# Kernel optimization log

Measured on AMD Instinct MI355X. Metric: run time of the kernel, lower is better.

The kernel has to match this reference:

```python
import jax, jax.numpy as jnp
import numpy as np

N_NODES = 100000
N_EDGES = 1600000
NUM_FEATURES = 512
HIDDEN = 128
NUM_CLASSES = 40


def setup_inputs() -> dict:
    key = jax.random.key(0)
    ks = jax.random.split(key, 6)
    x = jax.random.normal(ks[0], (N_NODES, NUM_FEATURES), dtype=jnp.float32)
    edge_index = jax.random.randint(ks[1], (2, N_EDGES), 0, N_NODES, dtype=jnp.int32)
    W1 = jax.random.normal(ks[2], (NUM_FEATURES, HIDDEN), dtype=jnp.float32) * 0.05
    b1 = jnp.zeros((HIDDEN,), dtype=jnp.float32)
    W2 = jax.random.normal(ks[3], (HIDDEN, NUM_CLASSES), dtype=jnp.float32) * 0.05
    b2 = jnp.zeros((NUM_CLASSES,), dtype=jnp.float32)
    return {"x": x, "edge_index": edge_index, "W1": W1, "b1": b1, "W2": W2, "b2": b2}


def _gcn_conv(x, W, b, src, dst, n):
    # PyG GCNConv: h = W x; out = D^{-1/2} (A + I) D^{-1/2} h + b
    h = x @ W                                            # [N, out]
    deg = jax.ops.segment_sum(jnp.ones(src.shape[0], h.dtype), dst,
                              num_segments=n) + 1.0      # +1 for self loop
    inv_sqrt = jax.lax.rsqrt(deg)                        # [N]
    coef = inv_sqrt[src] * inv_sqrt[dst]                 # [E]
    msgs = h[src] * coef[:, None]                        # [E, out] gather
    agg = jax.ops.segment_sum(msgs, dst, num_segments=n) # scatter-add
    agg = agg + h * (inv_sqrt * inv_sqrt)[:, None]       # self-loop term
    return agg + b


def reference(x, edge_index, W1, b1, W2, b2):
    src, dst = edge_index[0], edge_index[1]
    n = x.shape[0]
    h = jax.nn.relu(_gcn_conv(x, W1, b1, src, dst, n))
    # F.dropout(training=self.training): eval mode -> identity
    out = _gcn_conv(h, W2, b2, src, dst, n)
    return jax.nn.log_softmax(out, axis=1)
```

## Files before the change

kernel.cpp:

```cpp
#include <hip/hip_runtime.h>
#include <hip/hip_bf16.h>
#include <math.h>

#define N_NODES 100000
#define N_EDGES 1600000
#define F_IN 512
#define HID 128
#define NCLS 40
#define DEG_CAP 64
#define GM 128
#define NGB 782

typedef __attribute__((ext_vector_type(8))) short short8;
typedef __attribute__((ext_vector_type(4))) float floatx4;

__device__ __forceinline__ unsigned short f2bf(float x) {
    unsigned u = __builtin_bit_cast(unsigned, x);
    unsigned r = (u + 0x7FFFu + ((u >> 16) & 1u)) >> 16;
    return (unsigned short)r;
}
__device__ __forceinline__ float bflo(unsigned u) {
    return __builtin_bit_cast(float, u << 16);
}
__device__ __forceinline__ float bfhi(unsigned u) {
    return __builtin_bit_cast(float, u & 0xFFFF0000u);
}
__device__ __forceinline__ float dinv(int dg) {
    return rsqrtf((float)dg + 1.0f);
}


__global__ __launch_bounds__(256) void k_prep(
    const float* __restrict__ W1, unsigned short* __restrict__ W1t,
    const float* __restrict__ W2, unsigned short* __restrict__ W2th,
    unsigned short* __restrict__ W2tl, int* __restrict__ cursor) {
    int b = blockIdx.x;
    if (b < 256) {
        int idx = b * 256 + threadIdx.x;
        int n = idx >> 9, k = idx & 511;
        W1t[idx] = f2bf(W1[k * HID + n]);
    } else if (b < 280) {
        int idx = (b - 256) * 256 + threadIdx.x;
        int n = idx >> 7, k = idx & 127;
        float v = (n < NCLS) ? W2[k * NCLS + n] : 0.f;
        unsigned short hi = f2bf(v);
        unsigned short lo = f2bf(v - bflo(hi));
        W2th[idx] = hi;
        W2tl[idx] = lo;
    } else {
        int i = (b - 280) * 256 + threadIdx.x;
        if (i < N_NODES) cursor[i] = 0;
    }
}


__global__ __launch_bounds__(256) void k_fused_g1f(
    const float* __restrict__ A,
    const unsigned short* __restrict__ Bt,
    unsigned short* __restrict__ C,
    int M,
    const int* __restrict__ src, const int* __restrict__ dst,
    int* __restrict__ cursor, int* __restrict__ csr)
{
    __shared__ unsigned short Asl[128 * 40];
    __shared__ unsigned short Bsl[128 * 40];

    if (blockIdx.x >= NGB) {
        int i = (blockIdx.x - NGB) * 256 + threadIdx.x;
        int d = dst[i];
        int pos = atomicAdd(&cursor[d], 1);
        if (pos < DEG_CAP) csr[((size_t)d << 6) + pos] = src[i];
        return;
    }

    const int tid  = threadIdx.x;
    const int wave = tid >> 6;
    const int lane = tid & 63;
    const int quad = lane >> 4;
    const int l15  = lane & 15;
    const int wm   = (wave >> 1) * 64;
    const int wn   = (wave & 1) * 64;
    const int block_m = blockIdx.x * GM;

    floatx4 acc[4][4];
    #pragma unroll
    for (int i = 0; i < 4; ++i)
        #pragma unroll
        for (int j = 0; j < 4; ++j) acc[i][j] = (floatx4){0.f, 0.f, 0.f, 0.f};

    for (int k0 = 0; k0 < F_IN; k0 += 32) {
        #pragma unroll
        for (int i = 0; i < 4; ++i) {
            int f  = tid + 256 * i;
            int r  = f >> 3;
            int kq = f & 7;
            int gr = block_m + r;
            gr = gr < M ? gr : M - 1;
            floatx4 v = *(const floatx4*)&A[(size_t)gr * F_IN + k0 + kq * 4];
            unsigned lo = (unsigned)f2bf(v.x) | ((unsigned)f2bf(v.y) << 16);
            unsigned hi = (unsigned)f2bf(v.z) | ((unsigned)f2bf(v.w) << 16);
            *(uint2*)&Asl[r * 40 + kq * 4] = make_uint2(lo, hi);
        }
        #pragma unroll
        for (int i = 0; i < 2; ++i) {
            int f  = tid + 256 * i;
            int r  = f >> 2;
            int kq = f & 3;
            int4 v = *(const int4*)&Bt[(size_t)r * F_IN + k0 + kq * 8];
            *(int4*)&Bsl[r * 40 + kq * 8] = v;
        }
        __syncthreads();

        short8 af[4], bfr[4];
        #pragma unroll
        for (int t = 0; t < 4; ++t)
            af[t] = *(const short8*)&Asl[(wm + t * 16 + l15) * 40 + quad * 8];
        #pragma unroll
        for (int t = 0; t < 4; ++t)
            bfr[t] = *(const short8*)&Bsl[(wn + t * 16 + l15) * 40 + quad * 8];

        #pragma unroll
        for (int tm = 0; tm < 4; ++tm)
            #pragma unroll
            for (int tn = 0; tn < 4; ++tn)
                acc[tm][tn] = __builtin_amdgcn_mfma_f32_16x16x32_bf16(
                    af[tm], bfr[tn], acc[tm][tn], 0, 0, 0);
        __syncthreads();
    }

    #pragma unroll
    for (int tm = 0; tm < 4; ++tm) {
        #pragma unroll
        for (int r = 0; r < 4; ++r) {
            int row = block_m + wm + tm * 16 + quad * 4 + r;
            if (row < M) {
                #pragma unroll
                for (int tn = 0; tn < 4; ++tn)
                    C[(size_t)row * HID + wn + tn * 16 + l15] =
                        f2bf(acc[tm][tn][r]);
            }
        }
    }
}


__global__ __launch_bounds__(256) void k_gather1(
    const unsigned* __restrict__ h1s,
    const int* __restrict__ deg,
    const int* __restrict__ csr,
    const float* __restrict__ b1, float* __restrict__ hrelu)
{
    const int wave = threadIdx.x >> 6;
    const int lane = threadIdx.x & 63;
    const int node = blockIdx.x * 4 + wave;
    const int start = node << 6;
    const int dgn = deg[node];
    const float invd = dinv(dgn);
    int cnt = dgn < DEG_CAP ? dgn : DEG_CAP;

    unsigned u = h1s[(size_t)node * 64 + lane];
    float acc0 = bflo(u) * invd, acc1 = bfhi(u) * invd;

    int t = 0;
    for (; t + 16 <= cnt; t += 16) {
        int4 ia = *(const int4*)&csr[start + t];
        int4 ib = *(const int4*)&csr[start + t + 4];
        int4 ic = *(const int4*)&csr[start + t + 8];
        int4 id = *(const int4*)&csr[start + t + 12];
        float w0 = dinv(deg[ia.x]), w1 = dinv(deg[ia.y]);
        float w2 = dinv(deg[ia.z]), w3 = dinv(deg[ia.w]);
        float w4 = dinv(deg[ib.x]), w5 = dinv(deg[ib.y]);
        float w6 = dinv(deg[ib.z]), w7 = dinv(deg[ib.w]);
        float w8 = dinv(deg[ic.x]), w9 = dinv(deg[ic.y]);
        float wa = dinv(deg[ic.z]), wb = dinv(deg[ic.w]);
        float wc = dinv(deg[id.x]), wd = dinv(deg[id.y]);
        float we = dinv(deg[id.z]), wf = dinv(deg[id.w]);
        unsigned u0 = h1s[(size_t)ia.x * 64 + lane];
        unsigned u1 = h1s[(size_t)ia.y * 64 + lane];
        unsigned u2 = h1s[(size_t)ia.z * 64 + lane];
        unsigned u3 = h1s[(size_t)ia.w * 64 + lane];
        unsigned u4 = h1s[(size_t)ib.x * 64 + lane];
        unsigned u5 = h1s[(size_t)ib.y * 64 + lane];
        unsigned u6 = h1s[(size_t)ib.z * 64 + lane];
        unsigned u7 = h1s[(size_t)ib.w * 64 + lane];
        unsigned u8 = h1s[(size_t)ic.x * 64 + lane];
        unsigned u9 = h1s[(size_t)ic.y * 64 + lane];
        unsigned ua = h1s[(size_t)ic.z * 64 + lane];
        unsigned ub = h1s[(size_t)ic.w * 64 + lane];
        unsigned uc = h1s[(size_t)id.x * 64 + lane];
        unsigned ud = h1s[(size_t)id.y * 64 + lane];
        unsigned ue = h1s[(size_t)id.z * 64 + lane];
        unsigned uf = h1s[(size_t)id.w * 64 + lane];
        acc0 += (bflo(u0) * w0 + bflo(u1) * w1) + (bflo(u2) * w2 + bflo(u3) * w3);
        acc1 += (bfhi(u0) * w0 + bfhi(u1) * w1) + (bfhi(u2) * w2 + bfhi(u3) * w3);
        acc0 += (bflo(u4) * w4 + bflo(u5) * w5) + (bflo(u6) * w6 + bflo(u7) * w7);
        acc1 += (bfhi(u4) * w4 + bfhi(u5) * w5) + (bfhi(u6) * w6 + bfhi(u7) * w7);
        acc0 += (bflo(u8) * w8 + bflo(u9) * w9) + (bflo(ua) * wa + bflo(ub) * wb);
        acc1 += (bfhi(u8) * w8 + bfhi(u9) * w9) + (bfhi(ua) * wa + bfhi(ub) * wb);
        acc0 += (bflo(uc) * wc + bflo(ud) * wd) + (bflo(ue) * we + bflo(uf) * wf);
        acc1 += (bfhi(uc) * wc + bfhi(ud) * wd) + (bfhi(ue) * we + bfhi(uf) * wf);
    }
    for (; t + 8 <= cnt; t += 8) {
        int4 ia = *(const int4*)&csr[start + t];
        int4 ib = *(const int4*)&csr[start + t + 4];
        float w0 = dinv(deg[ia.x]), w1 = dinv(deg[ia.y]);
        float w2 = dinv(deg[ia.z]), w3 = dinv(deg[ia.w]);
        float w4 = dinv(deg[ib.x]), w5 = dinv(deg[ib.y]);
        float w6 = dinv(deg[ib.z]), w7 = dinv(deg[ib.w]);
        unsigned u0 = h1s[(size_t)ia.x * 64 + lane];
        unsigned u1 = h1s[(size_t)ia.y * 64 + lane];
        unsigned u2 = h1s[(size_t)ia.z * 64 + lane];
        unsigned u3 = h1s[(size_t)ia.w * 64 + lane];
        unsigned u4 = h1s[(size_t)ib.x * 64 + lane];
        unsigned u5 = h1s[(size_t)ib.y * 64 + lane];
        unsigned u6 = h1s[(size_t)ib.z * 64 + lane];
        unsigned u7 = h1s[(size_t)ib.w * 64 + lane];
        acc0 += (bflo(u0) * w0 + bflo(u1) * w1) + (bflo(u2) * w2 + bflo(u3) * w3);
        acc1 += (bfhi(u0) * w0 + bfhi(u1) * w1) + (bfhi(u2) * w2 + bfhi(u3) * w3);
        acc0 += (bflo(u4) * w4 + bflo(u5) * w5) + (bflo(u6) * w6 + bflo(u7) * w7);
        acc1 += (bfhi(u4) * w4 + bfhi(u5) * w5) + (bfhi(u6) * w6 + bfhi(u7) * w7);
    }
    for (; t + 4 <= cnt; t += 4) {
        int4 ia = *(const int4*)&csr[start + t];
        float w0 = dinv(deg[ia.x]), w1 = dinv(deg[ia.y]);
        float w2 = dinv(deg[ia.z]), w3 = dinv(deg[ia.w]);
        unsigned u0 = h1s[(size_t)ia.x * 64 + lane];
        unsigned u1 = h1s[(size_t)ia.y * 64 + lane];
        unsigned u2 = h1s[(size_t)ia.z * 64 + lane];
        unsigned u3 = h1s[(size_t)ia.w * 64 + lane];
        acc0 += (bflo(u0) * w0 + bflo(u1) * w1) + (bflo(u2) * w2 + bflo(u3) * w3);
        acc1 += (bfhi(u0) * w0 + bfhi(u1) * w1) + (bfhi(u2) * w2 + bfhi(u3) * w3);
    }
    for (; t < cnt; ++t) {
        int s = csr[start + t];
        float w = dinv(deg[s]);
        unsigned uu = h1s[(size_t)s * 64 + lane];
        acc0 += bflo(uu) * w;
        acc1 += bfhi(uu) * w;
    }

    float2 b = *(const float2*)&b1[lane * 2];
    float v0 = fmaxf(acc0 * invd + b.x, 0.f);
    float v1 = fmaxf(acc1 * invd + b.y, 0.f);
    *(float2*)&hrelu[(size_t)node * HID + lane * 2] = make_float2(v0, v1);
}


#define G2M 128

__global__ __launch_bounds__(256) void k_gemm2_mfma(
    const float* __restrict__ H,
    const unsigned short* __restrict__ Bh,
    const unsigned short* __restrict__ Bl,
    const int* __restrict__ deg,
    unsigned short* __restrict__ C,
    int M)
{
    __shared__ unsigned short Ahs[128 * 40];
    __shared__ unsigned short Als[128 * 40];
    __shared__ unsigned short Bhs[48 * 136];
    __shared__ unsigned short Bls[48 * 136];

    const int tid  = threadIdx.x;
    const int wave = tid >> 6;
    const int lane = tid & 63;
    const int quad = lane >> 4;
    const int l15  = lane & 15;
    const int wm   = wave * 32;
    const int block_m = blockIdx.x * G2M;

    for (int i = tid; i < 768; i += 256) {
        int n = i >> 4;
        int k = (i & 15) * 8;
        *(int4*)&Bhs[n * 136 + k] = *(const int4*)&Bh[n * 128 + k];
        *(int4*)&Bls[n * 136 + k] = *(const int4*)&Bl[n * 128 + k];
    }

    const int ra = tid >> 3, kqa = tid & 7;
    size_t aoff[4];
    #pragma unroll
    for (int i = 0; i < 4; ++i) {
        int gr = block_m + ra + 32 * i;
        gr = gr < M ? gr : M - 1;
        aoff[i] = (size_t)gr * HID + kqa * 4;
    }

    floatx4 hreg[4];
    #pragma unroll
    for (int i = 0; i < 4; ++i) hreg[i] = *(const floatx4*)&H[aoff[i]];

    floatx4 acc[2][3];
    #pragma unroll
    for (int i = 0; i < 2; ++i)
        #pragma unroll
        for (int j = 0; j < 3; ++j) acc[i][j] = (floatx4){0.f, 0.f, 0.f, 0.f};

    for (int step = 0; step < 4; ++step) {
        #pragma unroll
        for (int i = 0; i < 4; ++i) {
            floatx4 v = hreg[i];
            unsigned short hx = f2bf(v.x), hy = f2bf(v.y);
            unsigned short hz = f2bf(v.z), hw = f2bf(v.w);
            unsigned short lx = f2bf(v.x - bflo(hx));
            unsigned short ly = f2bf(v.y - bflo(hy));
            unsigned short lz = f2bf(v.z - bflo(hz));
            unsigned short lw = f2bf(v.w - bflo(hw));
            *(uint2*)&Ahs[(ra + 32 * i) * 40 + kqa * 4] =
                make_uint2((unsigned)hx | ((unsigned)hy << 16),
                           (unsigned)hz | ((unsigned)hw << 16));
            *(uint2*)&Als[(ra + 32 * i) * 40 + kqa * 4] =
                make_uint2((unsigned)lx | ((unsigned)ly << 16),
                           (unsigned)lz | ((unsigned)lw << 16));
        }
        __syncthreads();

        if (step < 3) {
            const int k1 = (step + 1) * 32;
            #pragma unroll
            for (int i = 0; i < 4; ++i) hreg[i] = *(const floatx4*)&H[aoff[i] + k1];
        }

        const int k0 = step * 32;
        short8 ah[2], al[2], bh[3], bl[3];
        #pragma unroll
        for (int t = 0; t < 2; ++t) {
            ah[t] = *(const short8*)&Ahs[(wm + t * 16 + l15) * 40 + quad * 8];
            al[t] = *(const short8*)&Als[(wm + t * 16 + l15) * 40 + quad * 8];
        }
        #pragma unroll
        for (int t = 0; t < 3; ++t) {
            bh[t] = *(const short8*)&Bhs[(t * 16 + l15) * 136 + k0 + quad * 8];
            bl[t] = *(const short8*)&Bls[(t * 16 + l15) * 136 + k0 + quad * 8];
        }

        #pragma unroll
        for (int tm = 0; tm < 2; ++tm)
            #pragma unroll
            for (int tn = 0; tn < 3; ++tn) {
                acc[tm][tn] = __builtin_amdgcn_mfma_f32_16x16x32_bf16(
                    ah[tm], bh[tn], acc[tm][tn], 0, 0, 0);
                acc[tm][tn] = __builtin_amdgcn_mfma_f32_16x16x32_bf16(
                    al[tm], bh[tn], acc[tm][tn], 0, 0, 0);
                acc[tm][tn] = __builtin_amdgcn_mfma_f32_16x16x32_bf16(
                    ah[tm], bl[tn], acc[tm][tn], 0, 0, 0);
            }
        __syncthreads();
    }

    #pragma unroll
    for (int tm = 0; tm < 2; ++tm) {
        #pragma unroll
        for (int r = 0; r < 4; ++r) {
            int row = block_m + wm + tm * 16 + quad * 4 + r;
            if (row < M) {
                float iv = dinv(deg[row]);
                #pragma unroll
                for (int tn = 0; tn < 3; ++tn) {
                    int col = tn * 16 + l15;
                    if (col < NCLS)
                        C[(size_t)row * NCLS + col] = f2bf(acc[tm][tn][r] * iv);
                }
            }
        }
    }
}


__global__ __launch_bounds__(256) void k_gather2(
    const unsigned* __restrict__ h2s,
    const int* __restrict__ deg,
    const int* __restrict__ csr,
    const float* __restrict__ b2, float* __restrict__ out)
{
    const int wave = threadIdx.x >> 6;
    const int lane = threadIdx.x & 63;
    const int node = blockIdx.x * 4 + wave;
    const int g = lane / 20;
    const int j = lane - g * 20;
    const int start = node << 6;
    const int dgn = deg[node];
    int cnt = dgn < DEG_CAP ? dgn : DEG_CAP;

    float acc0 = 0.f, acc1 = 0.f;
    if (g == 0) {
        unsigned u = h2s[(size_t)node * 20 + j];
        acc0 = bflo(u);
        acc1 = bfhi(u);
    }
    if (g < 3) {
        int t = g;
        for (; t + 9 < cnt; t += 12) {
            int s0 = csr[start + t];
            int s1 = csr[start + t + 3];
            int s2 = csr[start + t + 6];
            int s3 = csr[start + t + 9];
            unsigned u0 = h2s[(size_t)s0 * 20 + j];
            unsigned u1 = h2s[(size_t)s1 * 20 + j];
            unsigned u2 = h2s[(size_t)s2 * 20 + j];
            unsigned u3 = h2s[(size_t)s3 * 20 + j];
            acc0 += bflo(u0) + bflo(u1);
            acc1 += bfhi(u0) + bfhi(u1);
            acc0 += bflo(u2) + bflo(u3);
            acc1 += bfhi(u2) + bfhi(u3);
        }
        for (; t + 3 < cnt; t += 6) {
            int s0 = csr[start + t];
            int s1 = csr[start + t + 3];
            unsigned u0 = h2s[(size_t)s0 * 20 + j];
            unsigned u1 = h2s[(size_t)s1 * 20 + j];
            acc0 += bflo(u0) + bflo(u1);
            acc1 += bfhi(u0) + bfhi(u1);
        }
        if (t < cnt) {
            int s = csr[start + t];
            unsigned u = h2s[(size_t)s * 20 + j];
            acc0 += bflo(u);
            acc1 += bfhi(u);
        }
    }
    acc0 += __shfl(acc0, j + 20) + __shfl(acc0, j + 40);
    acc1 += __shfl(acc1, j + 20) + __shfl(acc1, j + 40);

    float invd = dinv(dgn);
    float v0 = -INFINITY, v1 = -INFINITY;
    if (g == 0) {
        float2 b = *(const float2*)&b2[j * 2];
        v0 = acc0 * invd + b.x;
        v1 = acc1 * invd + b.y;
    }
    float m = fmaxf(v0, v1);
    #pragma unroll
    for (int mask = 16; mask; mask >>= 1) m = fmaxf(m, __shfl_xor(m, mask));
    float e = (g == 0) ? (__expf(v0 - m) + __expf(v1 - m)) : 0.f;
    #pragma unroll
    for (int mask = 16; mask; mask >>= 1) e += __shfl_xor(e, mask);
    if (g == 0) {
        float lg = __logf(e);
        *(float2*)&out[(size_t)node * NCLS + j * 2] =
            make_float2(v0 - m - lg, v1 - m - lg);
    }
}


extern "C" void kernel_launch(void* const* d_in, const int* in_sizes, int n_in,
                              void* d_out, int out_size, void* d_ws, size_t ws_size,
                              hipStream_t stream) {
    const float* x   = (const float*)d_in[0];
    const int*   ei  = (const int*)d_in[1];
    const float* W1  = (const float*)d_in[2];
    const float* b1  = (const float*)d_in[3];
    const float* W2  = (const float*)d_in[4];
    const float* b2  = (const float*)d_in[5];
    float* out = (float*)d_out;

    const int* src = ei;
    const int* dst = ei + N_EDGES;

    char* wsb = (char*)d_ws;
    float* slot1    = (float*)wsb;
    float* hrelu    = slot1 + (size_t)N_NODES * HID;
    int*   cursor   = (int*)(hrelu + (size_t)N_NODES * HID);
    int*   csr_pad  = cursor + 131072;
    unsigned short* W1t  = (unsigned short*)(csr_pad + (size_t)N_NODES * DEG_CAP);
    unsigned short* W2th = W1t + (size_t)F_IN * HID;
    unsigned short* W2tl = W2th + 48 * 128;
    unsigned short* h1s_st = (unsigned short*)slot1;
    unsigned short* h2s_st = (unsigned short*)slot1;
    unsigned* h1s_ld = (unsigned*)slot1;
    unsigned* h2s_ld = (unsigned*)slot1;

    const int T = 256;
    const int NB = (N_NODES + 255) / 256;

    k_prep<<<280 + NB, T, 0, stream>>>(W1, W1t, W2, W2th, W2tl, cursor);

    k_fused_g1f<<<NGB + N_EDGES / T, T, 0, stream>>>(
        x, W1t, h1s_st, N_NODES, src, dst, cursor, csr_pad);

    k_gather1<<<N_NODES / 4, T, 0, stream>>>(h1s_ld, cursor, csr_pad, b1, hrelu);

    k_gemm2_mfma<<<(N_NODES + G2M - 1) / G2M, T, 0, stream>>>(hrelu, W2th, W2tl, cursor, h2s_st, N_NODES);
    k_gather2<<<N_NODES / 4, T, 0, stream>>>(h2s_ld, cursor, csr_pad, b2, out);
}
```

Measured before the change: 508.5 us.

## Split CSR build into 8 cursor slices and compact per node afterwards

Edge scatter now uses eight separate per-node cursor arrays chosen by block index, each with a 16-slot sub-bucket, so concurrent atomics on the same destination spread over different addresses. A new compaction kernel uses wave ballots to pack the valid entries of each node's 128-slot row and sums the slice counts into a degree array. This is meant to cut atomic contention in the CSR build, at the cost of an extra kernel launch, twice the CSR footprint and an 8x larger cursor initialisation. The per-slice cap of 16 could drop edges on skewed degree distributions.

```diff
diff --git a/kernel.cpp b/kernel.cpp
--- a/kernel.cpp
+++ b/kernel.cpp
@@ -7,9 +7,11 @@
 #define F_IN 512
 #define HID 128
 #define NCLS 40
-#define DEG_CAP 64
 #define GM 128
 #define NGB 782
+#define NFB 6250
+#define SCAP 16
+#define CUR_N 131072
 
 typedef __attribute__((ext_vector_type(8))) short short8;
 typedef __attribute__((ext_vector_type(4))) float floatx4;
@@ -33,7 +35,7 @@
 __global__ __launch_bounds__(256) void k_prep(
     const float* __restrict__ W1, unsigned short* __restrict__ W1t,
     const float* __restrict__ W2, unsigned short* __restrict__ W2th,
-    unsigned short* __restrict__ W2tl, int* __restrict__ cursor) {
+    unsigned short* __restrict__ W2tl, int* __restrict__ cur8) {
     int b = blockIdx.x;
     if (b < 256) {
         int idx = b * 256 + threadIdx.x;
@@ -49,7 +51,7 @@
         W2tl[idx] = lo;
     } else {
         int i = (b - 280) * 256 + threadIdx.x;
-        if (i < N_NODES) cursor[i] = 0;
+        cur8[i] = 0;
     }
 }
 
@@ -60,16 +62,18 @@
     unsigned short* __restrict__ C,
     int M,
     const int* __restrict__ src, const int* __restrict__ dst,
-    int* __restrict__ cursor, int* __restrict__ csr)
+    int* __restrict__ cur8, int* __restrict__ csr)
 {
     __shared__ unsigned short Asl[128 * 40];
     __shared__ unsigned short Bsl[128 * 40];
 
     if (blockIdx.x >= NGB) {
-        int i = (blockIdx.x - NGB) * 256 + threadIdx.x;
+        int fb = blockIdx.x - NGB;
+        int i = fb * 256 + threadIdx.x;
         int d = dst[i];
-        int pos = atomicAdd(&cursor[d], 1);
-        if (pos < DEG_CAP) csr[((size_t)d << 6) + pos] = src[i];
+        int s = fb & 7;
+        int pos = atomicAdd(&cur8[s * CUR_N + d], 1);
+        if (pos < SCAP) csr[((size_t)d << 7) + s * SCAP + pos] = src[i];
         return;
     }
 
@@ -144,6 +148,42 @@
 }
 
 
+__global__ __launch_bounds__(256) void k_compact(
+    const int* __restrict__ cur8, int* __restrict__ csr, int* __restrict__ deg)
+{
+    const int wave = threadIdx.x >> 6;
+    const int lane = threadIdx.x & 63;
+    const int node = blockIdx.x * 4 + wave;
+    const size_t base = (size_t)node << 7;
+
+    int k0 = lane, k1 = lane + 64;
+    int c0 = cur8[(k0 >> 4) * CUR_N + node];
+    int c1 = cur8[(k1 >> 4) * CUR_N + node];
+    c0 = c0 < SCAP ? c0 : SCAP;
+    c1 = c1 < SCAP ? c1 : SCAP;
+    bool ok0 = (k0 & 15) < c0;
+    bool ok1 = (k1 & 15) < c1;
+
+    int v0 = csr[base + k0];
+    unsigned long long m0 = __ballot(ok0);
+    int nA = __popcll(m0);
+    int p0 = __popcll(m0 & ((1ull << lane) - 1ull));
+    if (ok0) csr[base + p0] = v0;
+
+    int v1 = csr[base + k1];
+    unsigned long long m1 = __ballot(ok1);
+    int p1 = __popcll(m1 & ((1ull << lane) - 1ull));
+    if (ok1) csr[base + nA + p1] = v1;
+
+    if (lane == 0) {
+        int dsum = 0;
+        #pragma unroll
+        for (int s = 0; s < 8; ++s) dsum += cur8[s * CUR_N + node];
+        deg[node] = dsum;
+    }
+}
+
+
 __global__ __launch_bounds__(256) void k_gather1(
     const unsigned* __restrict__ h1s,
     const int* __restrict__ deg,
@@ -153,10 +193,10 @@
     const int wave = threadIdx.x >> 6;
     const int lane = threadIdx.x & 63;
     const int node = blockIdx.x * 4 + wave;
-    const int start = node << 6;
+    const int start = node << 7;
     const int dgn = deg[node];
     const float invd = dinv(dgn);
-    int cnt = dgn < DEG_CAP ? dgn : DEG_CAP;
+    int cnt = dgn < 128 ? dgn : 128;
 
     unsigned u = h1s[(size_t)node * 64 + lane];
     float acc0 = bflo(u) * invd, acc1 = bfhi(u) * invd;
@@ -377,9 +417,9 @@
     const int node = blockIdx.x * 4 + wave;
     const int g = lane / 20;
     const int j = lane - g * 20;
-    const int start = node << 6;
+    const int start = node << 7;
     const int dgn = deg[node];
-    int cnt = dgn < DEG_CAP ? dgn : DEG_CAP;
+    int cnt = dgn < 128 ? dgn : 128;
 
     float acc0 = 0.f, acc1 = 0.f;
     if (g == 0) {
@@ -459,9 +499,10 @@
     char* wsb = (char*)d_ws;
     float* slot1    = (float*)wsb;
     float* hrelu    = slot1 + (size_t)N_NODES * HID;
-    int*   cursor   = (int*)(hrelu + (size_t)N_NODES * HID);
-    int*   csr_pad  = cursor + 131072;
-    unsigned short* W1t  = (unsigned short*)(csr_pad + (size_t)N_NODES * DEG_CAP);
+    int*   deg      = (int*)(hrelu + (size_t)N_NODES * HID);
+    int*   cur8     = deg + CUR_N;
+    int*   csr_pad  = cur8 + 8 * CUR_N;
+    unsigned short* W1t  = (unsigned short*)(csr_pad + ((size_t)N_NODES << 7));
     unsigned short* W2th = W1t + (size_t)F_IN * HID;
     unsigned short* W2tl = W2th + 48 * 128;
     unsigned short* h1s_st = (unsigned short*)slot1;
@@ -470,15 +511,16 @@
     unsigned* h2s_ld = (unsigned*)slot1;
 
     const int T = 256;
-    const int NB = (N_NODES + 255) / 256;
-
-    k_prep<<<280 + NB, T, 0, stream>>>(W1, W1t, W2, W2th, W2tl, cursor);
-
-    k_fused_g1f<<<NGB + N_EDGES / T, T, 0, stream>>>(
-        x, W1t, h1s_st, N_NODES, src, dst, cursor, csr_pad);
-
-    k_gather1<<<N_NODES / 4, T, 0, stream>>>(h1s_ld, cursor, csr_pad, b1, hrelu);
-
-    k_gemm2_mfma<<<(N_NODES + G2M - 1) / G2M, T, 0, stream>>>(hrelu, W2th, W2tl, cursor, h2s_st, N_NODES);
-    k_gather2<<<N_NODES / 4, T, 0, stream>>>(h2s_ld, cursor, csr_pad, b2, out);
-}
+
+    k_prep<<<280 + (8 * CUR_N) / T, T, 0, stream>>>(W1, W1t, W2, W2th, W2tl, cur8);
+
+    k_fused_g1f<<<NGB + NFB, T, 0, stream>>>(
+        x, W1t, h1s_st, N_NODES, src, dst, cur8, csr_pad);
+
+    k_compact<<<N_NODES / 4, T, 0, stream>>>(cur8, csr_pad, deg);
+
+    k_gather1<<<N_NODES / 4, T, 0, stream>>>(h1s_ld, deg, csr_pad, b1, hrelu);
+
+    k_gemm2_mfma<<<(N_NODES + G2M - 1) / G2M, T, 0, stream>>>(hrelu, W2th, W2tl, deg, h2s_st, N_NODES);
+    k_gather2<<<N_NODES / 4, T, 0, stream>>>(h2s_ld, deg, csr_pad, b2, out);
+}
```

New measurement: 575.1 us. +13.1%, slower.
